# Kernel tuning notes

Measured on AMD Instinct MI355X. Metric: run time of the kernel, lower is better.

The kernel has to match this reference:

```python
import jax, jax.numpy as jnp
import numpy as np

EPS = 1e-07


def setup_inputs() -> dict:
    key = jax.random.key(0)
    k1, k2, k3 = jax.random.split(key, 3)
    B, C, H, W, K = 4, 64, 512, 512, 19
    x = jax.random.normal(k1, (B, C, H, W), dtype=jnp.float32)
    gt = jax.random.randint(k2, (B, H, W), 0, K, dtype=jnp.int32)
    aug_rand_info = jax.random.uniform(k3, (B, K, K), dtype=jnp.float32)
    return {"x": x, "gt": gt, "aug_rand_info": aug_rand_info}


def reference(x, gt, aug_rand_info):
    # x: [B,C,H,W], gt: [B,H,W] int labels in [0,K), aug_rand_info: [B,K,K]
    B, C, H, W = x.shape
    K = aug_rand_info.shape[1]
    HW = H * W
    # global segment id = b*K + class
    seg = (jnp.arange(B, dtype=jnp.int32)[:, None] * K + gt.reshape(B, HW)).reshape(-1)
    xf = x.reshape(B, C, HW).transpose(0, 2, 1).reshape(B * HW, C)  # [B*HW, C]
    # per-(image,class) sums and counts (segment reduce)
    sums = jax.ops.segment_sum(xf, seg, num_segments=B * K).reshape(B, K, C)
    cnt = jax.ops.segment_sum(jnp.ones((B * HW,), x.dtype), seg, num_segments=B * K).reshape(B, K, 1)
    valid = cnt > 0
    cnt_safe = jnp.where(valid, cnt, jnp.ones_like(cnt))
    mean = sums / cnt_safe                                     # [B,K,C]
    mean_px = mean.reshape(B * K, C)[seg]                      # gather per pixel
    var = jax.ops.segment_sum((xf - mean_px) ** 2, seg, num_segments=B * K).reshape(B, K, C) / cnt_safe
    std = jnp.sqrt(var) + EPS                                  # [B,K,C]
    # Dirichlet-style mixing weights over classes present in each image
    validf = valid.astype(x.dtype).reshape(B, 1, K)            # [B,1,K]
    w = aug_rand_info * validf                                 # zero out absent source classes
    w = w / jnp.clip(w.sum(-1, keepdims=True), EPS)            # renormalize -> simplex
    mix_mean = jnp.einsum('bck,bkd->bcd', w, mean)             # [B,K,C] style mean per target class
    mix_std = jnp.einsum('bck,bkd->bcd', w, std)
    # fused gather + per-class normalize + style scatter (class masks are disjoint)
    idx = gt.reshape(B, HW)[:, :, None]                        # [B,HW,1]
    take = lambda t: jnp.take_along_axis(t, idx, axis=1)       # [B,HW,C]
    m, s = take(mean), take(std)
    mm, ms = take(mix_mean), take(mix_std)
    xn = (xf.reshape(B, HW, C) - m) / s * ms + mm
    x_style = xn.transpose(0, 2, 1).reshape(B, C, H, W)
    return x_style
```

## Files before the change

### kernel.cpp

```cpp
#include <hip/hip_runtime.h>

#define EPSF 1e-7f

constexpr int Bn = 4, Cn = 64, Kn = 19;
constexpr int HWn = 512 * 512;

constexpr int SCH   = 128;
constexpr int SPIX  = HWn / SCH;
constexpr int SBLK  = 512;
constexpr int TSTR4 = 1028;
constexpr int PARTSZ = 2464;

typedef float f32x16_t __attribute__((ext_vector_type(16)));
typedef float f32x4_t  __attribute__((ext_vector_type(4)));
typedef short bf16x8_t __attribute__((ext_vector_type(8)));

#define PKBF(lo, hi) ((__builtin_bit_cast(unsigned, (hi)) & 0xFFFF0000u) | \
                      (__builtin_bit_cast(unsigned, (lo)) >> 16))

typedef const __attribute__((address_space(1))) void gas_void;
typedef __attribute__((address_space(3))) void las_void;

__device__ __forceinline__ void gload16(const float* g, float* l) {
    __builtin_amdgcn_global_load_lds((gas_void*)g, (las_void*)l, 16, 0, 0);
}

__global__ __launch_bounds__(SBLK, 4) void k_stats(
    const float* __restrict__ x, const int* __restrict__ gt,
    float* __restrict__ part)
{
    __shared__ float tile[16 * TSTR4];
    __shared__ int   lab[SPIX];
    __shared__ float credL[32];

    const int tid  = threadIdx.x;
    const int lane = tid & 63;
    const int w    = tid >> 6;
    const int g    = lane >> 5;
    const int col  = lane & 31;
    const int ch16 = col & 15;

    const int b    = blockIdx.x >> 7;
    const int pix0 = (blockIdx.x & 127) * SPIX;
    const float* xb  = x  + (size_t)b * Cn * HWn + pix0;
    const int*   gtb = gt + (size_t)b * HWn + pix0;

    {
        const int4 v = *reinterpret_cast<const int4*>(gtb + tid * 4);
        int4 cl;
        cl.x = min(max(v.x, 0), Kn - 1); cl.y = min(max(v.y, 0), Kn - 1);
        cl.z = min(max(v.z, 0), Kn - 1); cl.w = min(max(v.w, 0), Kn - 1);
        *reinterpret_cast<int4*>(&lab[tid * 4]) = cl;
    }

    f32x16_t dG0 = (f32x16_t)0.f, dG1 = (f32x16_t)0.f;
    f32x16_t dG2 = (f32x16_t)0.f, dG3 = (f32x16_t)0.f;
    int cnt = 0;

#define STAGE_(CG, PH) { \
    _Pragma("unroll") \
    for (int cc = 0; cc < 2; ++cc) { \
        const int row = w * 2 + cc; \
        const float* src = xb + (size_t)((CG) * 16 + row) * HWn + (PH) * 1024 + lane * 4; \
        float* dst = &tile[row * TSTR4]; \
        _Pragma("unroll") \
        for (int seg = 0; seg < 4; ++seg) \
            gload16(src + seg * 256, dst + seg * 256); \
    } }

#define COMPUTE_(PH, D, CNTON) { \
    _Pragma("unroll 1") \
    for (int s = 0; s < 8; ++s) { \
        const int pg = w * 128 + s * 16 + 8 * g; \
        const float4 va = *reinterpret_cast<const float4*>(&tile[ch16 * TSTR4 + pg]); \
        const float4 vb = *reinterpret_cast<const float4*>(&tile[ch16 * TSTR4 + pg + 4]); \
        float v0 = va.x, v1 = va.y, v2 = va.z, v3 = va.w; \
        float v4 = vb.x, v5 = vb.y, v6 = vb.z, v7 = vb.w; \
        if (col >= 16) { v0 *= v0; v1 *= v1; v2 *= v2; v3 *= v3; \
                         v4 *= v4; v5 *= v5; v6 *= v6; v7 *= v7; } \
        uint4 bw; \
        bw.x = PKBF(v0, v1); bw.y = PKBF(v2, v3); \
        bw.z = PKBF(v4, v5); bw.w = PKBF(v6, v7); \
        const int4 L0 = *reinterpret_cast<const int4*>(&lab[(PH) * 1024 + pg]); \
        const int4 L1 = *reinterpret_cast<const int4*>(&lab[(PH) * 1024 + pg + 4]); \
        const bool e0 = (L0.x == col), e1 = (L0.y == col); \
        const bool e2 = (L0.z == col), e3 = (L0.w == col); \
        const bool e4 = (L1.x == col), e5 = (L1.y == col); \
        const bool e6 = (L1.z == col), e7 = (L1.w == col); \
        int4 av; \
        av.x = (e0 ? 0x3F80u : 0u) | (e1 ? 0x3F800000u : 0u); \
        av.y = (e2 ? 0x3F80u : 0u) | (e3 ? 0x3F800000u : 0u); \
        av.z = (e4 ? 0x3F80u : 0u) | (e5 ? 0x3F800000u : 0u); \
        av.w = (e6 ? 0x3F80u : 0u) | (e7 ? 0x3F800000u : 0u); \
        if (CNTON) cnt += (int)e0 + (int)e1 + (int)e2 + (int)e3 \
                        + (int)e4 + (int)e5 + (int)e6 + (int)e7; \
        D = __builtin_amdgcn_mfma_f32_32x32x16_bf16( \
                __builtin_bit_cast(bf16x8_t, av), \
                __builtin_bit_cast(bf16x8_t, bw), D, 0, 0, 0); \
    } }

#define ROUND_(CG, PH, D, CNTON) \
    STAGE_(CG, PH) \
    __syncthreads(); \
    COMPUTE_(PH, D, CNTON) \
    __syncthreads();

    ROUND_(0, 0, dG0, true)
    ROUND_(1, 0, dG1, false)
    ROUND_(2, 0, dG2, false)
    ROUND_(3, 0, dG3, false)
    ROUND_(0, 1, dG0, true)
    ROUND_(1, 1, dG1, false)
    ROUND_(2, 1, dG2, false)
    ROUND_(3, 1, dG3, false)

    const int cnt2 = cnt + __shfl(cnt, col + 32, 64);

    float* redf = tile;
    const int statO = (col >> 4) * 64;
#define RED_(R, D, OP) { \
    _Pragma("unroll") \
    for (int r = 0; r < 16; ++r) { \
        const int krow = (r & 3) + 8 * (r >> 2) + 4 * g; \
        if (krow < Kn) redf[krow * 128 + statO + (R) * 16 + ch16] OP D[r]; \
    } }
    #pragma unroll 1
    for (int ww = 0; ww < 8; ++ww) {
        if (w == ww) {
            if (ww == 0) { RED_(0, dG0, =)  RED_(1, dG1, =)  RED_(2, dG2, =)  RED_(3, dG3, =) }
            else         { RED_(0, dG0, +=) RED_(1, dG1, +=) RED_(2, dG2, +=) RED_(3, dG3, +=) }
            if (lane < Kn) {
                if (ww == 0) credL[lane]  = (float)cnt2;
                else         credL[lane] += (float)cnt2;
            }
        }
        __syncthreads();
    }

    float* pb = part + (size_t)blockIdx.x * PARTSZ;
    for (int i = tid; i < 2 * Cn * Kn; i += SBLK) {
        const int stat = i / (Cn * Kn);
        const int rr   = i - stat * (Cn * Kn);
        const int c = rr / Kn, k = rr - c * Kn;
        pb[i] = redf[k * 128 + stat * 64 + c];
    }
    if (tid < Kn) pb[2 * Cn * Kn + tid] = credL[tid];
}

__global__ __launch_bounds__(1024) void k_tables(
    const float* __restrict__ part, const float* __restrict__ aug,
    float* __restrict__ tabAB)
{
    __shared__ float mean_s[Kn * Cn];
    __shared__ float std_s [Kn * Cn];
    __shared__ float wrow  [Kn * Kn];
    __shared__ float wsum  [Kn];
    __shared__ float validf[Kn], cntf[Kn];

    const int b = blockIdx.x, tid = threadIdx.x;
    const float* pbase = part + (size_t)b * SCH * PARTSZ;

    if (tid < Kn) {
        float s = 0.f;
        for (int blk = 0; blk < SCH; ++blk)
            s += pbase[(size_t)blk * PARTSZ + 2 * Cn * Kn + tid];
        validf[tid] = (s > 0.f) ? 1.f : 0.f;
        cntf[tid]   = (s > 0.f) ? s : 1.f;
    }
    __syncthreads();

    for (int i = tid; i < Cn * Kn; i += 1024) {
        float s = 0.f, q = 0.f;
        for (int blk = 0; blk < SCH; ++blk) {
            s += pbase[(size_t)blk * PARTSZ + i];
            q += pbase[(size_t)blk * PARTSZ + Cn * Kn + i];
        }
        const int c = i / Kn, k = i - c * Kn;
        const float cs  = cntf[k];
        const float m   = s / cs;
        const float var = fmaxf(q / cs - m * m, 0.f);
        mean_s[k * Cn + c] = m;
        std_s [k * Cn + c] = sqrtf(var) + EPSF;
    }
    for (int i = tid; i < Kn * Kn; i += 1024) {
        const int t = i / Kn, k = i - t * Kn;
        wrow[i] = aug[((size_t)b * Kn + t) * Kn + k] * validf[k];
    }
    __syncthreads();
    if (tid < Kn) {
        float s = 0.f;
        for (int k = 0; k < Kn; ++k) s += wrow[tid * Kn + k];
        wsum[tid] = fmaxf(s, EPSF);
    }
    __syncthreads();
    for (int i = tid; i < Kn * Cn; i += 1024) {
        const int t = i >> 6, c = i & 63;
        const float inv = 1.f / wsum[t];
        float mm = 0.f, ms = 0.f;
        for (int k = 0; k < Kn; ++k) {
            const float wk = wrow[t * Kn + k] * inv;
            mm += wk * mean_s[k * Cn + c];
            ms += wk * std_s [k * Cn + c];
        }
        const float A  = ms / std_s[t * Cn + c];
        const float Bv = mm - mean_s[t * Cn + c] * A;
        const size_t o = ((size_t)b * Cn * Kn + c * Kn + t) * 2;
        tabAB[o + 0] = A;
        tabAB[o + 1] = Bv;
    }
}

constexpr int ABLK = 1024;
constexpr int ACH  = 64;
constexpr int APIX = HWn / ACH;

__global__ __launch_bounds__(ABLK, 4) void k_apply(
    const float* __restrict__ x, const int* __restrict__ gt,
    const float* __restrict__ tabAB, float* __restrict__ out)
{
    __shared__ float ABs[Cn * Kn * 2];
    const int tid   = threadIdx.x;
    const int b     = blockIdx.x >> 6;
    const int chunk = blockIdx.x & 63;

    for (int i = tid; i < Cn * Kn * 2; i += ABLK)
        ABs[i] = tabAB[(size_t)b * Cn * Kn * 2 + i];
    __syncthreads();

    const int p0 = chunk * APIX + tid * 4;
    const int4 L = *reinterpret_cast<const int4*>(gt + (size_t)b * HWn + p0);
    const int l0 = min(max(L.x, 0), Kn - 1);
    const int l1 = min(max(L.y, 0), Kn - 1);
    const int l2 = min(max(L.z, 0), Kn - 1);
    const int l3 = min(max(L.w, 0), Kn - 1);

    const float* xp = x   + (size_t)b * Cn * HWn + p0;
    float*       op = out + (size_t)b * Cn * HWn + p0;

    #pragma unroll 4
    for (int c = 0; c < Cn; ++c) {
        const float4 v = *reinterpret_cast<const float4*>(xp + (size_t)c * HWn);
        const int co = c * Kn;
        const float2 ab0 = *reinterpret_cast<const float2*>(&ABs[(co + l0) * 2]);
        const float2 ab1 = *reinterpret_cast<const float2*>(&ABs[(co + l1) * 2]);
        const float2 ab2 = *reinterpret_cast<const float2*>(&ABs[(co + l2) * 2]);
        const float2 ab3 = *reinterpret_cast<const float2*>(&ABs[(co + l3) * 2]);
        float4 o;
        o.x = v.x * ab0.x + ab0.y;
        o.y = v.y * ab1.x + ab1.y;
        o.z = v.z * ab2.x + ab2.y;
        o.w = v.w * ab3.x + ab3.y;
        __builtin_nontemporal_store(__builtin_bit_cast(f32x4_t, o),
                                    reinterpret_cast<f32x4_t*>(op + (size_t)c * HWn));
    }
}

extern "C" void kernel_launch(void* const* d_in, const int* in_sizes, int n_in,
                              void* d_out, int out_size, void* d_ws, size_t ws_size,
                              hipStream_t stream) {
    const float* x   = (const float*)d_in[0];
    const int*   gt  = (const int*)d_in[1];
    const float* aug = (const float*)d_in[2];
    float* out = (float*)d_out;

    float* part  = (float*)d_ws;
    float* tabAB = part + (size_t)Bn * SCH * PARTSZ;

    k_stats <<<dim3(Bn * SCH), dim3(SBLK), 0, stream>>>(x, gt, part);
    k_tables<<<dim3(Bn),       dim3(1024), 0, stream>>>(part, aug, tabAB);
    k_apply <<<dim3(Bn * ACH), dim3(ABLK), 0, stream>>>(x, gt, tabAB, out);
}
```

Measured before the change: 174.5 us.

## Double-buffer LDS tiles in stats kernel to overlap global loads with MFMA

The stats kernel now uses two LDS tiles. It issues the async global-to-LDS load for the next channel group while computing on the current one, and drops one barrier per round. The aim is to hide global load latency inside each block rather than relying on other resident blocks. The cost is doubled LDS use (about 136KB per block), which likely limits each CU to one 512-thread block. The launch bound minimum blocks is lowered to match, so the loss of cross-block overlap may offset the gain.

```diff
diff --git a/kernel.cpp b/kernel.cpp
--- a/kernel.cpp
+++ b/kernel.cpp
@@ -25,11 +25,12 @@
     __builtin_amdgcn_global_load_lds((gas_void*)g, (las_void*)l, 16, 0, 0);
 }
 
-__global__ __launch_bounds__(SBLK, 4) void k_stats(
+__global__ __launch_bounds__(SBLK, 2) void k_stats(
     const float* __restrict__ x, const int* __restrict__ gt,
     float* __restrict__ part)
 {
-    __shared__ float tile[16 * TSTR4];
+    __shared__ float tileA[16 * TSTR4];
+    __shared__ float tileB[16 * TSTR4];
     __shared__ int   lab[SPIX];
     __shared__ float credL[32];
 
@@ -57,23 +58,23 @@
     f32x16_t dG2 = (f32x16_t)0.f, dG3 = (f32x16_t)0.f;
     int cnt = 0;
 
-#define STAGE_(CG, PH) { \
+#define STAGE_(BUF, CG, PH) { \
     _Pragma("unroll") \
     for (int cc = 0; cc < 2; ++cc) { \
         const int row = w * 2 + cc; \
         const float* src = xb + (size_t)((CG) * 16 + row) * HWn + (PH) * 1024 + lane * 4; \
-        float* dst = &tile[row * TSTR4]; \
+        float* dst = &BUF[row * TSTR4]; \
         _Pragma("unroll") \
         for (int seg = 0; seg < 4; ++seg) \
             gload16(src + seg * 256, dst + seg * 256); \
     } }
 
-#define COMPUTE_(PH, D, CNTON) { \
+#define COMPUTE_(BUF, PH, D, CNTON) { \
     _Pragma("unroll 1") \
     for (int s = 0; s < 8; ++s) { \
         const int pg = w * 128 + s * 16 + 8 * g; \
-        const float4 va = *reinterpret_cast<const float4*>(&tile[ch16 * TSTR4 + pg]); \
-        const float4 vb = *reinterpret_cast<const float4*>(&tile[ch16 * TSTR4 + pg + 4]); \
+        const float4 va = *reinterpret_cast<const float4*>(&BUF[ch16 * TSTR4 + pg]); \
+        const float4 vb = *reinterpret_cast<const float4*>(&BUF[ch16 * TSTR4 + pg + 4]); \
         float v0 = va.x, v1 = va.y, v2 = va.z, v3 = va.w; \
         float v4 = vb.x, v5 = vb.y, v6 = vb.z, v7 = vb.w; \
         if (col >= 16) { v0 *= v0; v1 *= v1; v2 *= v2; v3 *= v3; \
@@ -99,24 +100,20 @@
                 __builtin_bit_cast(bf16x8_t, bw), D, 0, 0, 0); \
     } }
 
-#define ROUND_(CG, PH, D, CNTON) \
-    STAGE_(CG, PH) \
-    __syncthreads(); \
-    COMPUTE_(PH, D, CNTON) \
-    __syncthreads();
-
-    ROUND_(0, 0, dG0, true)
-    ROUND_(1, 0, dG1, false)
-    ROUND_(2, 0, dG2, false)
-    ROUND_(3, 0, dG3, false)
-    ROUND_(0, 1, dG0, true)
-    ROUND_(1, 1, dG1, false)
-    ROUND_(2, 1, dG2, false)
-    ROUND_(3, 1, dG3, false)
+    STAGE_(tileA, 0, 0)
+    __syncthreads();
+    STAGE_(tileB, 1, 0)  COMPUTE_(tileA, 0, dG0, true)   __syncthreads();
+    STAGE_(tileA, 2, 0)  COMPUTE_(tileB, 0, dG1, false)  __syncthreads();
+    STAGE_(tileB, 3, 0)  COMPUTE_(tileA, 0, dG2, false)  __syncthreads();
+    STAGE_(tileA, 0, 1)  COMPUTE_(tileB, 0, dG3, false)  __syncthreads();
+    STAGE_(tileB, 1, 1)  COMPUTE_(tileA, 1, dG0, true)   __syncthreads();
+    STAGE_(tileA, 2, 1)  COMPUTE_(tileB, 1, dG1, false)  __syncthreads();
+    STAGE_(tileB, 3, 1)  COMPUTE_(tileA, 1, dG2, false)  __syncthreads();
+                         COMPUTE_(tileB, 1, dG3, false)  __syncthreads();
 
     const int cnt2 = cnt + __shfl(cnt, col + 32, 64);
 
-    float* redf = tile;
+    float* redf = tileA;
     const int statO = (col >> 4) * 64;
 #define RED_(R, D, OP) { \
     _Pragma("unroll") \
```

Result: slower. 190.4 us (+9.1%).
